# Kernel optimization log

Measured on AMD Instinct MI355X. Metric: run time of the kernel, lower is better.

Reference implementation:

```python
import jax, jax.numpy as jnp
import numpy as np

TOP_K = 2  # matches init_kwargs top_k


def setup_inputs() -> dict:
    key = jax.random.key(0)
    ks = jax.random.split(key, 7)
    d_model, d_ff, E = 512, 2048, 8
    B, S = 2, 2048
    std = 0.02
    return {
        "x": jax.random.normal(ks[0], (B, S, d_model), dtype=jnp.float32),
        "Wr": jax.random.normal(ks[1], (E, d_model), dtype=jnp.float32) * std,
        "br": jnp.zeros((E,), dtype=jnp.float32),
        "W1": jax.random.normal(ks[2], (E, d_model, d_ff), dtype=jnp.float32) * (1.0 / np.sqrt(d_model)),
        "b1": jnp.zeros((E, d_ff), dtype=jnp.float32),
        "W2": jax.random.normal(ks[3], (E, d_ff, d_model), dtype=jnp.float32) * (1.0 / np.sqrt(d_ff)),
        "b2": jnp.zeros((E, d_model), dtype=jnp.float32),
    }


def _moe_forward(x, Wr, br, W1, b1, W2, b2):
    leading = x.shape[:-1]
    d = x.shape[-1]
    E = Wr.shape[0]
    xf = x.reshape(-1, d)                                   # [N, d]
    N = xf.shape[0]

    # --- token router (linear head) ---
    logits = xf @ Wr.T + br                                  # [N, E]
    routing = jax.nn.softmax(logits, axis=-1)                # [N, E]
    sel_w, sel_idx = jax.lax.top_k(routing, TOP_K)           # [N, K]
    sel_w = sel_w / jnp.sum(sel_w, axis=-1, keepdims=True)   # renormalize top-k

    # combine weights as dense [N, E] (zero for unselected experts)
    combine = jnp.zeros((N, E), dtype=xf.dtype).at[
        jnp.arange(N)[:, None], sel_idx
    ].add(sel_w)                                             # [N, E]

    # --- expert FFNs (dense all-expert compute, masked combine) ---
    h = jax.nn.gelu(jnp.einsum("nd,edf->enf", xf, W1) + b1[:, None, :])  # [E, N, ff]
    y = jnp.einsum("enf,efd->end", h, W2) + b2[:, None, :]               # [E, N, d]

    out = jnp.einsum("ne,end->nd", combine, y)               # [N, d]
    return out.reshape(*leading, d)


def reference(x, Wr, br, W1, b1, W2, b2):
    return _moe_forward(x, Wr, br, W1, b1, W2, b2)
```

## Files before the change

### kernel.cpp

```cpp
#include <hip/hip_runtime.h>
#include <hip/hip_bf16.h>
#include <cstdint>

typedef unsigned short u16;
typedef __bf16 bf16_t;
typedef __bf16 bf16x8 __attribute__((ext_vector_type(8)));
typedef float f32x4 __attribute__((ext_vector_type(4)));

#define DM   512
#define DFF  2048
#define NEXP 8

__device__ __forceinline__ u16 f2bf(float f) {
  bf16_t b = (bf16_t)f;
  return __builtin_bit_cast(u16, b);
}
__device__ __forceinline__ uint32_t pack_bf2(float lo, float hi) {
  return (uint32_t)f2bf(lo) | ((uint32_t)f2bf(hi) << 16);
}
__device__ __forceinline__ float gelu_tanh(float x) {
  float x3 = x * x * x;
  float z = 0.7978845608028654f * (x + 0.044715f * x3);
  float az = fabsf(z);
  float e = __expf(2.0f * az);
  float t = 1.0f - 2.0f / (e + 1.0f);
  t = copysignf(t, z);
  return 0.5f * x * (1.0f + t);
}
__device__ __forceinline__ void async16(const u16* g, u16* l) {
  __builtin_amdgcn_global_load_lds((const __attribute__((address_space(1))) void*)g,
                                   (__attribute__((address_space(3))) void*)l, 16, 0, 0);
}

__global__ void k_transpose_cvt(const float* __restrict__ src, u16* __restrict__ dst,
                                int R, int C) {
  __shared__ u16 tile[64][66];
  int e = blockIdx.y;
  int tilesC = C >> 6;
  int bR = (blockIdx.x / tilesC) << 6;
  int bC = (blockIdx.x % tilesC) << 6;
  const float* s = src + (size_t)e * R * C;
  u16* d = dst + (size_t)e * R * C;
  int rr = threadIdx.x >> 4;
  int cc = (threadIdx.x & 15) << 2;
#pragma unroll
  for (int i = 0; i < 4; ++i) {
    int r = (i << 4) + rr;
    float4 v = *(const float4*)(s + (size_t)(bR + r) * C + bC + cc);
    *(uint32_t*)&tile[r][cc]     = pack_bf2(v.x, v.y);
    *(uint32_t*)&tile[r][cc + 2] = pack_bf2(v.z, v.w);
  }
  __syncthreads();
  int c0 = threadIdx.x >> 5;
  int j  = (threadIdx.x & 31) << 1;
#pragma unroll
  for (int i = 0; i < 8; ++i) {
    int c = (i << 3) + c0;
    uint32_t v = (uint32_t)tile[j][c] | ((uint32_t)tile[j + 1][c] << 16);
    *(uint32_t*)(&d[(size_t)(bC + c) * R + bR + j]) = v;
  }
}

__global__ void k_router(const float* __restrict__ x, const float* __restrict__ Wr,
                         const float* __restrict__ br, int* __restrict__ sel_idx,
                         float* __restrict__ sel_w, int Ntok) {
  int wid = threadIdx.x >> 6;
  int lane = threadIdx.x & 63;
  int tok = (blockIdx.x << 2) + wid;
  if (tok >= Ntok) return;
  const float4* xr = (const float4*)(x + (size_t)tok * DM);
  float4 x0 = xr[lane * 2], x1 = xr[lane * 2 + 1];
  float logit[NEXP];
#pragma unroll
  for (int e = 0; e < NEXP; ++e) {
    const float4* wr = (const float4*)(Wr + e * DM);
    float4 w0 = wr[lane * 2], w1 = wr[lane * 2 + 1];
    float p = x0.x * w0.x + x0.y * w0.y + x0.z * w0.z + x0.w * w0.w
            + x1.x * w1.x + x1.y * w1.y + x1.z * w1.z + x1.w * w1.w;
#pragma unroll
    for (int off = 32; off; off >>= 1) p += __shfl_xor(p, off, 64);
    logit[e] = p + br[e];
  }
  if (lane == 0) {
    float mx = logit[0];
#pragma unroll
    for (int e = 1; e < NEXP; ++e) mx = fmaxf(mx, logit[e]);
    float pr[NEXP];
#pragma unroll
    for (int e = 0; e < NEXP; ++e) pr[e] = __expf(logit[e] - mx);
    int i0 = 0;
#pragma unroll
    for (int e = 1; e < NEXP; ++e) if (pr[e] > pr[i0]) i0 = e;
    int i1 = -1;
#pragma unroll
    for (int e = 0; e < NEXP; ++e) {
      if (e == i0) continue;
      if (i1 < 0 || pr[e] > pr[i1]) i1 = e;
    }
    float s2 = pr[i0] + pr[i1];
    sel_idx[tok * 2]     = i0;
    sel_idx[tok * 2 + 1] = i1;
    sel_w[tok * 2]       = pr[i0] / s2;
    sel_w[tok * 2 + 1]   = pr[i1] / s2;
  }
}

__global__ void k_scatter(const int* __restrict__ sel_idx, const float* __restrict__ sel_w,
                          int npairs, int* __restrict__ row_token, float* __restrict__ row_w,
                          int* __restrict__ pos_of, int* __restrict__ tileMeta,
                          int* __restrict__ gMeta) {
  __shared__ int cnt[NEXP], offs[NEXP], cur[NEXP];
  int tid = threadIdx.x;
  int lane = tid & 63;
  if (tid < NEXP) { cnt[tid] = 0; cur[tid] = 0; }
  __syncthreads();
  for (int p = tid; p < npairs; p += blockDim.x) {
    int e = sel_idx[p];
#pragma unroll
    for (int ex = 0; ex < NEXP; ++ex) {
      unsigned long long m = __ballot(e == ex);
      if (lane == 0 && m) atomicAdd(&cnt[ex], __popcll(m));
    }
  }
  __syncthreads();
  if (tid == 0) {
    int o = 0, nmt = 0;
    for (int e = 0; e < NEXP; ++e) {
      offs[e] = o;
      int c = cnt[e];
      int nt = (c + 127) >> 7;
      for (int t = 0; t < nt; ++t) {
        tileMeta[nmt * 3 + 0] = o + t * 128;
        tileMeta[nmt * 3 + 1] = o + c;
        tileMeta[nmt * 3 + 2] = e;
        ++nmt;
      }
      o += c;
    }
    gMeta[0] = nmt;
  }
  __syncthreads();
  for (int p = tid; p < npairs; p += blockDim.x) {
    int e = sel_idx[p];
    int pos = 0;
#pragma unroll
    for (int ex = 0; ex < NEXP; ++ex) {
      unsigned long long m = __ballot(e == ex);
      if (m) {
        int leader = __ffsll((long long)m) - 1;
        int base = 0;
        if (lane == leader) base = atomicAdd(&cur[ex], __popcll(m));
        base = __shfl(base, leader, 64);
        if (e == ex)
          pos = offs[ex] + base + __popcll(m & ((1ull << lane) - 1ull));
      }
    }
    row_token[pos] = p >> 1;
    row_w[pos] = sel_w[p];
    pos_of[p] = pos;
  }
}

__global__ void k_gather(const float* __restrict__ x, const int* __restrict__ row_token,
                         u16* __restrict__ Xg, int npairs) {
  int pos = (blockIdx.x << 2) + (threadIdx.x >> 6);
  int lane = threadIdx.x & 63;
  if (pos >= npairs) return;
  int tok = row_token[pos];
  const float4* src = (const float4*)(x + (size_t)tok * DM);
  float4 a = src[lane * 2], b = src[lane * 2 + 1];
  uint4 o;
  o.x = pack_bf2(a.x, a.y);
  o.y = pack_bf2(a.z, a.w);
  o.z = pack_bf2(b.x, b.y);
  o.w = pack_bf2(b.z, b.w);
  ((uint4*)(Xg + (size_t)pos * DM))[lane] = o;
}

template <int NFULL, int KTOT, int KCHUNK, bool GELU, bool SCALE, bool OUTBF16>
__launch_bounds__(256)
__global__ void k_gemm(const u16* __restrict__ A, const u16* __restrict__ BT,
                       const float* __restrict__ bias, const float* __restrict__ row_w,
                       void* __restrict__ Out, size_t pstride,
                       const int* __restrict__ tileMeta, const int* __restrict__ gMeta,
                       int maxmt) {
  constexpr int NT = NFULL / 128;
  constexpr int NK = KCHUNK / 32;
  int NB = gridDim.x;
  int bid = blockIdx.x;
  int wg = ((NB & 7) == 0) ? ((bid & 7) * (NB >> 3) + (bid >> 3)) : bid;
  int nt = wg % NT;
  int rem = wg / NT;
  int mt = rem % maxmt;
  int split = rem / maxmt;
  if (mt >= gMeta[0]) return;
  int posStart = tileMeta[mt * 3 + 0];
  int segEnd   = tileMeta[mt * 3 + 1];
  int e        = tileMeta[mt * 3 + 2];

  __shared__ __align__(16) u16 smem[24576];

  int tid = threadIdx.x, lane = tid & 63, wid = tid >> 6;
  int wm = wid >> 1, wn = wid & 1;

  const u16* Abase = A + (size_t)split * KCHUNK;
  const u16* Bbase = BT + ((size_t)e * NFULL + (size_t)nt * 128) * KTOT + (size_t)split * KCHUNK;

  int l4 = lane >> 2, c4 = lane & 3;
  const u16* aS[2];
  const u16* bS[2];
#pragma unroll
  for (int i = 0; i < 2; ++i) {
    int r = i * 64 + wid * 16 + l4;
    int gra = posStart + r;
    if (gra >= segEnd) gra = segEnd - 1;
    int cs = c4 ^ ((r >> 1) & 3);
    aS[i] = Abase + (size_t)gra * KTOT + cs * 8;
    bS[i] = Bbase + (size_t)r * KTOT + cs * 8;
  }

  auto stage = [&](int kt, int buf) {
    u16* as = smem + buf * 8192;
    u16* bs = as + 4096;
#pragma unroll
    for (int i = 0; i < 2; ++i) {
      async16(aS[i] + kt * 32, as + i * 2048 + wid * 512);
      async16(bS[i] + kt * 32, bs + i * 2048 + wid * 512);
    }
  };

  f32x4 acc[4][4] = {};

  stage(0, 0);
  stage(1, 1);
  int bufC = 0, bufS = 2;
#pragma unroll 1
  for (int t = 0; t < NK; ++t) {
    if (t + 1 < NK) asm volatile("s_waitcnt vmcnt(4)" ::: "memory");
    else            asm volatile("s_waitcnt vmcnt(0)" ::: "memory");
    __builtin_amdgcn_s_barrier();
    asm volatile("" ::: "memory");
    if (t + 2 < NK) { stage(t + 2, bufS); bufS = (bufS == 2) ? 0 : bufS + 1; }
    const char* AsB = (const char*)(smem + bufC * 8192);
    const char* BsB = AsB + 8192;
    int kb = (lane >> 4) << 4;
    bf16x8 av[4], bv[4];
#pragma unroll
    for (int mi = 0; mi < 4; ++mi) {
      int row = (wm << 6) + (mi << 4) + (lane & 15);
      av[mi] = *(const bf16x8*)(AsB + row * 64 + (kb ^ (((row >> 1) & 3) << 4)));
    }
#pragma unroll
    for (int ni = 0; ni < 4; ++ni) {
      int row = (wn << 6) + (ni << 4) + (lane & 15);
      bv[ni] = *(const bf16x8*)(BsB + row * 64 + (kb ^ (((row >> 1) & 3) << 4)));
    }
    __builtin_amdgcn_s_setprio(1);
#pragma unroll
    for (int mi = 0; mi < 4; ++mi)
#pragma unroll
      for (int ni = 0; ni < 4; ++ni)
        acc[mi][ni] = __builtin_amdgcn_mfma_f32_16x16x32_bf16(av[mi], bv[ni], acc[mi][ni], 0, 0, 0);
    __builtin_amdgcn_s_setprio(0);
    bufC = (bufC == 2) ? 0 : bufC + 1;
  }

  int laneCol = lane & 15;
  int laneRow4 = (lane >> 4) << 2;
  const float* biasE = bias + (size_t)e * NFULL;

  if constexpr (OUTBF16) {
    __syncthreads();
    u16* Cs = smem;
#pragma unroll
    for (int mi = 0; mi < 4; ++mi) {
#pragma unroll
      for (int j = 0; j < 4; ++j) {
        int r = (wm << 6) + (mi << 4) + laneRow4 + j;
#pragma unroll
        for (int ni = 0; ni < 4; ++ni) {
          int cl = (wn << 6) + (ni << 4) + laneCol;
          float v = acc[mi][ni][j] + biasE[(nt << 7) + cl];
          if constexpr (GELU) v = gelu_tanh(v);
          Cs[r * 136 + cl] = f2bf(v);
        }
      }
    }
    __syncthreads();
    int r0 = tid >> 4, q = tid & 15;
    u16* OutU = (u16*)Out;
#pragma unroll
    for (int i = 0; i < 8; ++i) {
      int r = (i << 4) + r0;
      if (posStart + r < segEnd)
        *((uint4*)(OutU + (size_t)(posStart + r) * NFULL + (nt << 7)) + q) =
            ((uint4*)(Cs + (size_t)r * 136))[q];
    }
  } else {
    float* OutF = (float*)Out + (size_t)split * pstride;
#pragma unroll
    for (int mi = 0; mi < 4; ++mi) {
#pragma unroll
      for (int j = 0; j < 4; ++j) {
        int m = posStart + (wm << 6) + (mi << 4) + laneRow4 + j;
        if (m < segEnd) {
          float w = 1.0f;
          if constexpr (SCALE) w = row_w[m];
#pragma unroll
          for (int ni = 0; ni < 4; ++ni) {
            int n = (nt << 7) + (wn << 6) + (ni << 4) + laneCol;
            float v = acc[mi][ni][j] + (split == 0 ? biasE[n] : 0.0f);
            OutF[(size_t)m * NFULL + n] = v * w;
          }
        }
      }
    }
  }
}

__global__ void k_combine(const float* __restrict__ P, size_t pstride,
                          const int* __restrict__ pos_of, float* __restrict__ out, int Ntok) {
  int tok = (blockIdx.x << 2) + (threadIdx.x >> 6);
  int lane = threadIdx.x & 63;
  if (tok >= Ntok) return;
  int p0 = pos_of[tok * 2], p1 = pos_of[tok * 2 + 1];
  const float4* a0 = (const float4*)(P + (size_t)p0 * DM);
  const float4* a1 = (const float4*)(P + pstride + (size_t)p0 * DM);
  const float4* b0 = (const float4*)(P + (size_t)p1 * DM);
  const float4* b1 = (const float4*)(P + pstride + (size_t)p1 * DM);
  float4* o = (float4*)(out + (size_t)tok * DM);
#pragma unroll
  for (int i = 0; i < 2; ++i) {
    int idx = lane * 2 + i;
    float4 x0 = a0[idx], x1 = a1[idx], y0 = b0[idx], y1 = b1[idx];
    o[idx] = make_float4(x0.x + x1.x + y0.x + y1.x,
                         x0.y + x1.y + y0.y + y1.y,
                         x0.z + x1.z + y0.z + y1.z,
                         x0.w + x1.w + y0.w + y1.w);
  }
}

extern "C" void kernel_launch(void* const* d_in, const int* in_sizes, int n_in,
                              void* d_out, int out_size, void* d_ws, size_t ws_size,
                              hipStream_t stream) {
  const float* x  = (const float*)d_in[0];
  const float* Wr = (const float*)d_in[1];
  const float* br = (const float*)d_in[2];
  const float* W1 = (const float*)d_in[3];
  const float* b1 = (const float*)d_in[4];
  const float* W2 = (const float*)d_in[5];
  const float* b2 = (const float*)d_in[6];
  float* out = (float*)d_out;

  int Ntok = in_sizes[0] / DM;
  int npairs = Ntok * 2;
  int maxmt = npairs / 128 + NEXP;
  size_t pstride = (size_t)npairs * DM;

  char* p = (char*)d_ws;
  u16* W1T = (u16*)p;  p += (size_t)NEXP * DFF * DM * 2;
  u16* W2T = (u16*)p;  p += (size_t)NEXP * DM * DFF * 2;
  u16* Xg  = (u16*)p;  p += (size_t)npairs * DM * 2;
  u16* H   = (u16*)p;  p += (size_t)npairs * DFF * 2;
  float* Part = (float*)p; p += 2 * pstride * 4;
  int* sel_idx   = (int*)p;   p += (size_t)npairs * 4;
  float* sel_w   = (float*)p; p += (size_t)npairs * 4;
  int* pos_of    = (int*)p;   p += (size_t)npairs * 4;
  int* row_token = (int*)p;   p += (size_t)npairs * 4;
  float* row_w   = (float*)p; p += (size_t)npairs * 4;
  int* tileMeta  = (int*)p;   p += (size_t)(maxmt * 3 + 16) * 4;
  int* gMeta     = (int*)p;   p += 64;

  k_transpose_cvt<<<dim3((DM / 64) * (DFF / 64), NEXP), 256, 0, stream>>>(W1, W1T, DM, DFF);
  k_transpose_cvt<<<dim3((DFF / 64) * (DM / 64), NEXP), 256, 0, stream>>>(W2, W2T, DFF, DM);
  k_router<<<dim3((Ntok + 3) / 4), 256, 0, stream>>>(x, Wr, br, sel_idx, sel_w, Ntok);
  k_scatter<<<dim3(1), 1024, 0, stream>>>(sel_idx, sel_w, npairs, row_token, row_w,
                                          pos_of, tileMeta, gMeta);
  k_gather<<<dim3(npairs / 4), 256, 0, stream>>>(x, row_token, Xg, npairs);
  k_gemm<DFF, DM, DM, true, false, true>
      <<<dim3(maxmt * (DFF / 128)), 256, 0, stream>>>(
          Xg, W1T, b1, nullptr, H, 0, tileMeta, gMeta, maxmt);
  k_gemm<DM, DFF, DFF / 2, false, true, false>
      <<<dim3(maxmt * (DM / 128) * 2), 256, 0, stream>>>(
          H, W2T, b2, row_w, Part, pstride, tileMeta, gMeta, maxmt);
  k_combine<<<dim3(Ntok / 4), 256, 0, stream>>>(Part, pstride, pos_of, out, Ntok);
}
```

Baseline: 144.4 us.

## Fuse prep kernels, store split-K partials as bf16, add supertile block ordering

Three weight-transpose/router launches are merged into one k_prep kernel dispatched by block index, removing launch overhead and tail gaps. The second GEMM now writes its split-K partials as bf16 through the shared-memory staged epilogue instead of scattered fp32 stores, halving partial-buffer traffic, and k_combine reads bf16. The GEMM block index is remapped into 8-row supertiles so neighbouring blocks share weight tiles in cache. Storing partials in bf16 adds rounding error to the output.

```diff
diff --git a/kernel.cpp b/kernel.cpp
--- a/kernel.cpp
+++ b/kernel.cpp
@@ -32,15 +32,13 @@
                                    (__attribute__((address_space(3))) void*)l, 16, 0, 0);
 }
 
-__global__ void k_transpose_cvt(const float* __restrict__ src, u16* __restrict__ dst,
-                                int R, int C) {
+__device__ __forceinline__ void transpose_tile(const float* __restrict__ s,
+                                               u16* __restrict__ d, int R, int C,
+                                               int tileIdx) {
   __shared__ u16 tile[64][66];
-  int e = blockIdx.y;
   int tilesC = C >> 6;
-  int bR = (blockIdx.x / tilesC) << 6;
-  int bC = (blockIdx.x % tilesC) << 6;
-  const float* s = src + (size_t)e * R * C;
-  u16* d = dst + (size_t)e * R * C;
+  int bR = (tileIdx / tilesC) << 6;
+  int bC = (tileIdx % tilesC) << 6;
   int rr = threadIdx.x >> 4;
   int cc = (threadIdx.x & 15) << 2;
 #pragma unroll
@@ -61,12 +59,26 @@
   }
 }
 
-__global__ void k_router(const float* __restrict__ x, const float* __restrict__ Wr,
-                         const float* __restrict__ br, int* __restrict__ sel_idx,
-                         float* __restrict__ sel_w, int Ntok) {
+__global__ void k_prep(const float* __restrict__ W1, u16* __restrict__ W1T,
+                       const float* __restrict__ W2, u16* __restrict__ W2T,
+                       const float* __restrict__ x, const float* __restrict__ Wr,
+                       const float* __restrict__ br, int* __restrict__ sel_idx,
+                       float* __restrict__ sel_w, int Ntok) {
+  int b = blockIdx.x;
+  if (b < 2048) {
+    int e = b >> 8, t = b & 255;
+    transpose_tile(W1 + (size_t)e * DM * DFF, W1T + (size_t)e * DM * DFF, DM, DFF, t);
+    return;
+  }
+  if (b < 4096) {
+    int e = (b - 2048) >> 8, t = (b - 2048) & 255;
+    transpose_tile(W2 + (size_t)e * DFF * DM, W2T + (size_t)e * DFF * DM, DFF, DM, t);
+    return;
+  }
+  int rb = b - 4096;
   int wid = threadIdx.x >> 6;
   int lane = threadIdx.x & 63;
-  int tok = (blockIdx.x << 2) + wid;
+  int tok = (rb << 2) + wid;
   if (tok >= Ntok) return;
   const float4* xr = (const float4*)(x + (size_t)tok * DM);
   float4 x0 = xr[lane * 2], x1 = xr[lane * 2 + 1];
@@ -177,34 +189,42 @@
   ((uint4*)(Xg + (size_t)pos * DM))[lane] = o;
 }
 
-template <int NFULL, int KTOT, int KCHUNK, bool GELU, bool SCALE, bool OUTBF16>
+template <int NFULL, int KTOT, int NSPLIT, bool GELU, bool SCALE>
 __launch_bounds__(256)
 __global__ void k_gemm(const u16* __restrict__ A, const u16* __restrict__ BT,
                        const float* __restrict__ bias, const float* __restrict__ row_w,
-                       void* __restrict__ Out, size_t pstride,
+                       u16* __restrict__ Out, size_t pstride,
                        const int* __restrict__ tileMeta, const int* __restrict__ gMeta,
                        int maxmt) {
-  constexpr int NT = NFULL / 128;
-  constexpr int NK = KCHUNK / 32;
+  constexpr int NTN = NFULL / 128;
+  constexpr int SN  = (NTN >= 8) ? 8 : NTN;
+  constexpr int NSN = NTN / SN;
+  constexpr int SUPER = 8 * SN;
+  constexpr int KCH = KTOT / NSPLIT;
+  constexpr int NK  = KCH / 32;
+
+  __shared__ __align__(16) u16 smem[24576];
+
   int NB = gridDim.x;
   int bid = blockIdx.x;
   int wg = ((NB & 7) == 0) ? ((bid & 7) * (NB >> 3) + (bid >> 3)) : bid;
-  int nt = wg % NT;
-  int rem = wg / NT;
-  int mt = rem % maxmt;
-  int split = rem / maxmt;
+  int s = wg / SUPER, l = wg % SUPER;
+  int nsm = maxmt >> 3;
+  int split = s / (nsm * NSN);
+  int srem  = s % (nsm * NSN);
+  int sm = srem / NSN, sn = srem % NSN;
+  int mt = sm * 8 + l / SN;
+  int nt = sn * SN + l % SN;
   if (mt >= gMeta[0]) return;
   int posStart = tileMeta[mt * 3 + 0];
   int segEnd   = tileMeta[mt * 3 + 1];
   int e        = tileMeta[mt * 3 + 2];
 
-  __shared__ __align__(16) u16 smem[24576];
-
   int tid = threadIdx.x, lane = tid & 63, wid = tid >> 6;
   int wm = wid >> 1, wn = wid & 1;
 
-  const u16* Abase = A + (size_t)split * KCHUNK;
-  const u16* Bbase = BT + ((size_t)e * NFULL + (size_t)nt * 128) * KTOT + (size_t)split * KCHUNK;
+  const u16* Ab = A + (size_t)split * KCH;
+  const u16* Bb = BT + ((size_t)e * NFULL + (size_t)nt * 128) * KTOT + (size_t)split * KCH;
 
   int l4 = lane >> 2, c4 = lane & 3;
   const u16* aS[2];
@@ -212,15 +232,14 @@
 #pragma unroll
   for (int i = 0; i < 2; ++i) {
     int r = i * 64 + wid * 16 + l4;
-    int gra = posStart + r;
-    if (gra >= segEnd) gra = segEnd - 1;
+    int g = posStart + r; if (g >= segEnd) g = segEnd - 1;
     int cs = c4 ^ ((r >> 1) & 3);
-    aS[i] = Abase + (size_t)gra * KTOT + cs * 8;
-    bS[i] = Bbase + (size_t)r * KTOT + cs * 8;
-  }
-
-  auto stage = [&](int kt, int buf) {
-    u16* as = smem + buf * 8192;
+    aS[i] = Ab + (size_t)g * KTOT + cs * 8;
+    bS[i] = Bb + (size_t)r * KTOT + cs * 8;
+  }
+
+  auto stage = [&](int kt, int slot) {
+    u16* as = smem + slot * 8192;
     u16* bs = as + 4096;
 #pragma unroll
     for (int i = 0; i < 2; ++i) {
@@ -265,79 +284,61 @@
     bufC = (bufC == 2) ? 0 : bufC + 1;
   }
 
+  __syncthreads();
+  u16* Cs = smem;
   int laneCol = lane & 15;
   int laneRow4 = (lane >> 4) << 2;
   const float* biasE = bias + (size_t)e * NFULL;
-
-  if constexpr (OUTBF16) {
-    __syncthreads();
-    u16* Cs = smem;
-#pragma unroll
-    for (int mi = 0; mi < 4; ++mi) {
-#pragma unroll
-      for (int j = 0; j < 4; ++j) {
-        int r = (wm << 6) + (mi << 4) + laneRow4 + j;
-#pragma unroll
-        for (int ni = 0; ni < 4; ++ni) {
-          int cl = (wn << 6) + (ni << 4) + laneCol;
-          float v = acc[mi][ni][j] + biasE[(nt << 7) + cl];
-          if constexpr (GELU) v = gelu_tanh(v);
-          Cs[r * 136 + cl] = f2bf(v);
-        }
+  u16* OutS = Out + (size_t)split * pstride;
+#pragma unroll
+  for (int mi = 0; mi < 4; ++mi) {
+#pragma unroll
+    for (int j = 0; j < 4; ++j) {
+      int r = (wm << 6) + (mi << 4) + laneRow4 + j;
+      int m = posStart + r;
+      int mc = m < segEnd ? m : segEnd - 1;
+      float w = 1.0f;
+      if constexpr (SCALE) w = row_w[mc];
+#pragma unroll
+      for (int ni = 0; ni < 4; ++ni) {
+        int cl = (wn << 6) + (ni << 4) + laneCol;
+        float v = acc[mi][ni][j];
+        if (split == 0) v += biasE[nt * 128 + cl];
+        if constexpr (GELU) v = gelu_tanh(v);
+        if constexpr (SCALE) v *= w;
+        Cs[r * 136 + cl] = f2bf(v);
       }
     }
-    __syncthreads();
-    int r0 = tid >> 4, q = tid & 15;
-    u16* OutU = (u16*)Out;
-#pragma unroll
-    for (int i = 0; i < 8; ++i) {
-      int r = (i << 4) + r0;
-      if (posStart + r < segEnd)
-        *((uint4*)(OutU + (size_t)(posStart + r) * NFULL + (nt << 7)) + q) =
-            ((uint4*)(Cs + (size_t)r * 136))[q];
-    }
-  } else {
-    float* OutF = (float*)Out + (size_t)split * pstride;
-#pragma unroll
-    for (int mi = 0; mi < 4; ++mi) {
-#pragma unroll
-      for (int j = 0; j < 4; ++j) {
-        int m = posStart + (wm << 6) + (mi << 4) + laneRow4 + j;
-        if (m < segEnd) {
-          float w = 1.0f;
-          if constexpr (SCALE) w = row_w[m];
-#pragma unroll
-          for (int ni = 0; ni < 4; ++ni) {
-            int n = (nt << 7) + (wn << 6) + (ni << 4) + laneCol;
-            float v = acc[mi][ni][j] + (split == 0 ? biasE[n] : 0.0f);
-            OutF[(size_t)m * NFULL + n] = v * w;
-          }
-        }
-      }
-    }
-  }
-}
-
-__global__ void k_combine(const float* __restrict__ P, size_t pstride,
+  }
+  __syncthreads();
+  int r0 = tid >> 4, q = tid & 15;
+#pragma unroll
+  for (int i = 0; i < 8; ++i) {
+    int r = (i << 4) + r0;
+    if (posStart + r < segEnd)
+      *((uint4*)(OutS + (size_t)(posStart + r) * NFULL + (nt << 7)) + q) =
+          ((uint4*)(Cs + (size_t)r * 136))[q];
+  }
+}
+
+template <int NSPLIT>
+__global__ void k_combine(const u16* __restrict__ P, size_t pstride,
                           const int* __restrict__ pos_of, float* __restrict__ out, int Ntok) {
   int tok = (blockIdx.x << 2) + (threadIdx.x >> 6);
   int lane = threadIdx.x & 63;
   if (tok >= Ntok) return;
   int p0 = pos_of[tok * 2], p1 = pos_of[tok * 2 + 1];
-  const float4* a0 = (const float4*)(P + (size_t)p0 * DM);
-  const float4* a1 = (const float4*)(P + pstride + (size_t)p0 * DM);
-  const float4* b0 = (const float4*)(P + (size_t)p1 * DM);
-  const float4* b1 = (const float4*)(P + pstride + (size_t)p1 * DM);
-  float4* o = (float4*)(out + (size_t)tok * DM);
-#pragma unroll
-  for (int i = 0; i < 2; ++i) {
-    int idx = lane * 2 + i;
-    float4 x0 = a0[idx], x1 = a1[idx], y0 = b0[idx], y1 = b1[idx];
-    o[idx] = make_float4(x0.x + x1.x + y0.x + y1.x,
-                         x0.y + x1.y + y0.y + y1.y,
-                         x0.z + x1.z + y0.z + y1.z,
-                         x0.w + x1.w + y0.w + y1.w);
-  }
+  float s[8] = {};
+#pragma unroll
+  for (int sp = 0; sp < NSPLIT; ++sp) {
+    bf16x8 a = ((const bf16x8*)(P + sp * pstride + (size_t)p0 * DM))[lane];
+    bf16x8 b = ((const bf16x8*)(P + sp * pstride + (size_t)p1 * DM))[lane];
+#pragma unroll
+    for (int i = 0; i < 8; ++i) s[i] += (float)a[i] + (float)b[i];
+  }
+  float4* o = (float4*)(out + (size_t)tok * DM + lane * 8);
+  o[0] = make_float4(s[0], s[1], s[2], s[3]);
+  o[1] = make_float4(s[4], s[5], s[6], s[7]);
 }
 
 extern "C" void kernel_launch(void* const* d_in, const int* in_sizes, int n_in,
@@ -362,7 +363,7 @@
   u16* W2T = (u16*)p;  p += (size_t)NEXP * DM * DFF * 2;
   u16* Xg  = (u16*)p;  p += (size_t)npairs * DM * 2;
   u16* H   = (u16*)p;  p += (size_t)npairs * DFF * 2;
-  float* Part = (float*)p; p += 2 * pstride * 4;
+  u16* Part = (u16*)p; p += 2 * pstride * 2;
   int* sel_idx   = (int*)p;   p += (size_t)npairs * 4;
   float* sel_w   = (float*)p; p += (size_t)npairs * 4;
   int* pos_of    = (int*)p;   p += (size_t)npairs * 4;
@@ -371,17 +372,16 @@
   int* tileMeta  = (int*)p;   p += (size_t)(maxmt * 3 + 16) * 4;
   int* gMeta     = (int*)p;   p += 64;
 
-  k_transpose_cvt<<<dim3((DM / 64) * (DFF / 64), NEXP), 256, 0, stream>>>(W1, W1T, DM, DFF);
-  k_transpose_cvt<<<dim3((DFF / 64) * (DM / 64), NEXP), 256, 0, stream>>>(W2, W2T, DFF, DM);
-  k_router<<<dim3((Ntok + 3) / 4), 256, 0, stream>>>(x, Wr, br, sel_idx, sel_w, Ntok);
+  k_prep<<<dim3(4096 + Ntok / 4), 256, 0, stream>>>(W1, W1T, W2, W2T, x, Wr, br,
+                                                    sel_idx, sel_w, Ntok);
   k_scatter<<<dim3(1), 1024, 0, stream>>>(sel_idx, sel_w, npairs, row_token, row_w,
                                           pos_of, tileMeta, gMeta);
   k_gather<<<dim3(npairs / 4), 256, 0, stream>>>(x, row_token, Xg, npairs);
-  k_gemm<DFF, DM, DM, true, false, true>
+  k_gemm<DFF, DM, 1, true, false>
       <<<dim3(maxmt * (DFF / 128)), 256, 0, stream>>>(
           Xg, W1T, b1, nullptr, H, 0, tileMeta, gMeta, maxmt);
-  k_gemm<DM, DFF, DFF / 2, false, true, false>
+  k_gemm<DM, DFF, 2, false, true>
       <<<dim3(maxmt * (DM / 128) * 2), 256, 0, stream>>>(
           H, W2T, b2, row_w, Part, pstride, tileMeta, gMeta, maxmt);
-  k_combine<<<dim3(Ntok / 4), 256, 0, stream>>>(Part, pstride, pos_of, out, Ntok);
-}
+  k_combine<2><<<dim3(Ntok / 4), 256, 0, stream>>>(Part, pstride, pos_of, out, Ntok);
+}
```

After: 143.3 us. No clear change (-0.7%).
